# Kernel optimization log

Measured on AMD Instinct MI355X. Metric: run time of the kernel, lower is better.

Reference implementation:

```python
import jax, jax.numpy as jnp
import numpy as np
import math

D_MODEL = 1024
N_HEADS = 16
D_K = D_MODEL // N_HEADS


def setup_inputs() -> dict:
    key = jax.random.key(0)
    ks = jax.random.split(key, 9)
    s = 1.0 / math.sqrt(D_MODEL)
    x = jax.random.normal(ks[0], (2, 2048, D_MODEL), dtype=jnp.float32)
    # nn.Linear stores weight as [out, in]; we store transposed [in, out] for x @ W
    Wq = jax.random.uniform(ks[1], (D_MODEL, D_MODEL), jnp.float32, -s, s)
    bq = jax.random.uniform(ks[2], (D_MODEL,), jnp.float32, -s, s)
    Wk = jax.random.uniform(ks[3], (D_MODEL, D_MODEL), jnp.float32, -s, s)
    bk = jax.random.uniform(ks[4], (D_MODEL,), jnp.float32, -s, s)
    Wv = jax.random.uniform(ks[5], (D_MODEL, D_MODEL), jnp.float32, -s, s)
    bv = jax.random.uniform(ks[6], (D_MODEL,), jnp.float32, -s, s)
    Wo = jax.random.uniform(ks[7], (D_MODEL, D_MODEL), jnp.float32, -s, s)
    bo = jax.random.uniform(ks[8], (D_MODEL,), jnp.float32, -s, s)
    return {"x": x, "Wq": Wq, "bq": bq, "Wk": Wk, "bk": bk,
            "Wv": Wv, "bv": bv, "Wo": Wo, "bo": bo}


def reference(x, Wq, bq, Wk, bk, Wv, bv, Wo, bo):
    B, S, _ = x.shape
    scale = 1.0 / math.sqrt(D_K)
    # projections -> [B, H, S, Dk]
    def split_heads(t):
        return t.reshape(B, S, N_HEADS, D_K).transpose(0, 2, 1, 3)
    q = split_heads(x @ Wq + bq)
    k = split_heads(x @ Wk + bk)
    v = split_heads(x @ Wv + bv)
    # [B, H, S, S] scores
    scores = jnp.einsum('bhqd,bhkd->bhqk', q, k) * scale
    weights = jax.nn.softmax(scores, axis=-1)  # dropout p=0.0 -> identity
    attn = jnp.einsum('bhqk,bhkd->bhqd', weights, v)
    attn = attn.transpose(0, 2, 1, 3).reshape(B, S, D_MODEL)
    return attn @ Wo + bo
```

## Files before the change

kernel.cpp:

```cpp
#include <hip/hip_runtime.h>

#define DM    1024
#define NTOK  4096

typedef __attribute__((ext_vector_type(8))) short short8;
typedef __attribute__((ext_vector_type(4))) float floatx4;

__device__ __forceinline__ ushort f2bf(float f) {
  union { float f; uint32_t u; } v; v.f = f;
  uint32_t r = (v.u + 0x7fffu + ((v.u >> 16) & 1u)) >> 16;
  return (ushort)r;
}
__device__ __forceinline__ uint f2bf2(float a, float b) {
  return (uint)f2bf(a) | ((uint)f2bf(b) << 16);
}
__device__ __forceinline__ uint pkhi(float a, float b) {
  uint ua = __float_as_uint(a) + 0x8000u;
  uint ub = __float_as_uint(b) + 0x8000u;
  return __builtin_amdgcn_perm(ub, ua, 0x07060302);
}

__device__ __forceinline__ floatx4 mfma16(short8 a, short8 b, floatx4 c) {
  return __builtin_amdgcn_mfma_f32_16x16x32_bf16(a, b, c, 0, 0, 0);
}

__device__ __forceinline__ void glld16(const ushort* g, ushort* l) {
  __builtin_amdgcn_global_load_lds(
      (const __attribute__((address_space(1))) void*)g,
      (__attribute__((address_space(3))) void*)l, 16, 0, 0);
}

__device__ __forceinline__ void stage_slab(const ushort* gbase, int strideHW,
                                           ushort* lds, int ii, int lane) {
  const int r = ii * 8 + (lane >> 3);
  const int c = (lane & 7) ^ (r & 7);
  glld16(gbase + (size_t)r * strideHW + c * 8, lds + ii * 512);
}

__device__ __forceinline__ short8 fragr(const ushort* lds, int row, int chunk) {
  return *reinterpret_cast<const short8*>(&lds[row * 64 + ((chunk ^ (row & 7)) << 3)]);
}

__global__ __launch_bounds__(256) void k_prep(const float* __restrict__ x,
                                              const float* __restrict__ Wq,
                                              const float* __restrict__ Wk,
                                              const float* __restrict__ Wv,
                                              const float* __restrict__ Wo,
                                              ushort* __restrict__ xb,
                                              ushort* __restrict__ Wtout) {
  __shared__ float tile[32][33];
  const int bx = blockIdx.x, tid = threadIdx.x;
  if (bx < 2048) {
    int i = (bx * 256 + tid) * 8;
    float4 f0 = *reinterpret_cast<const float4*>(x + i);
    float4 f1 = *reinterpret_cast<const float4*>(x + i + 4);
    short8 o;
    o[0] = (short)f2bf(f0.x); o[1] = (short)f2bf(f0.y);
    o[2] = (short)f2bf(f0.z); o[3] = (short)f2bf(f0.w);
    o[4] = (short)f2bf(f1.x); o[5] = (short)f2bf(f1.y);
    o[6] = (short)f2bf(f1.z); o[7] = (short)f2bf(f1.w);
    *reinterpret_cast<short8*>(xb + i) = o;
    return;
  }
  const int idx = bx - 2048;
  const int z = idx >> 10, rem = idx & 1023;
  const float* W = (z == 0) ? Wq : (z == 1) ? Wk : (z == 2) ? Wv : Wo;
  ushort* Wt = Wtout + (size_t)z * (DM * DM);
  const int bxt = (rem & 31) * 32, byt = (rem >> 5) * 32;
  const int tx = tid & 31, ty = tid >> 5;
#pragma unroll
  for (int i = 0; i < 32; i += 8)
    tile[ty + i][tx] = W[(byt + ty + i) * DM + bxt + tx];
  __syncthreads();
#pragma unroll
  for (int i = 0; i < 32; i += 8)
    Wt[(bxt + ty + i) * DM + byt + tx] = f2bf(tile[tx][ty + i]);
}

__global__ __launch_bounds__(256) void k_gemm_qkv(const ushort* __restrict__ Am,
                                                  const ushort* __restrict__ Bm,
                                                  const float* __restrict__ bq,
                                                  const float* __restrict__ bk,
                                                  const float* __restrict__ bv,
                                                  ushort* __restrict__ Qo,
                                                  ushort* __restrict__ Ko,
                                                  ushort* __restrict__ Vto) {
  __shared__ ushort smem[32768];
  const int tid = threadIdx.x;
  const int w = tid >> 6, lane = tid & 63;
  const int quad = lane >> 4, l15 = lane & 15;
  const int wm = w >> 1, wn = w & 1;
  const int bm = blockIdx.x & 31, bn = blockIdx.x >> 5;
  const int sel = bn >> 3;
  const int bnl = bn & 7;

  const ushort* Ab = Am + (size_t)bm * 128 * 1024;
  const ushort* Bb = Bm + (size_t)bn * 128 * 1024;

  floatx4 acc[4][4] = {};

  auto stage = [&](int it, int buf) {
    ushort* As = smem + buf * 16384;
    ushort* Bs = As + 8192;
    const int k0 = it * 64;
#pragma unroll
    for (int i = 0; i < 4; ++i) stage_slab(Ab + k0, 1024, As, w * 4 + i, lane);
#pragma unroll
    for (int i = 0; i < 4; ++i) stage_slab(Bb + k0, 1024, Bs, w * 4 + i, lane);
  };

  stage(0, 0);
  for (int it = 0; it < 16; ++it) {
    __syncthreads();
    if (it + 1 < 16) stage(it + 1, (it + 1) & 1);
    const ushort* As = smem + (it & 1) * 16384;
    const ushort* Bs = As + 8192;
#pragma unroll
    for (int ks = 0; ks < 2; ++ks) {
      short8 af[4], bf[4];
#pragma unroll
      for (int t = 0; t < 4; ++t) {
        af[t] = fragr(As, wm * 64 + t * 16 + l15, ks * 4 + quad);
        bf[t] = fragr(Bs, wn * 64 + t * 16 + l15, ks * 4 + quad);
      }
#pragma unroll
      for (int tm = 0; tm < 4; ++tm)
#pragma unroll
        for (int tn = 0; tn < 4; ++tn)
          acc[tm][tn] = mfma16(af[tm], bf[tn], acc[tm][tn]);
    }
  }

  if (sel < 2) {
    const float* bp = sel ? bk : bq;
    ushort* dst = sel ? Ko : Qo;
    const float sc = sel ? 1.0f : 0.18033688f;
#pragma unroll
    for (int tm = 0; tm < 4; ++tm)
#pragma unroll
      for (int tn = 0; tn < 4; ++tn) {
        const int mg0 = bm * 128 + wm * 64 + tm * 16 + quad * 4;
        const int np = bnl * 128 + wn * 64 + tn * 16 + l15;
        const float bb = bp[np];
#pragma unroll
        for (int r = 0; r < 4; ++r) {
          const int m = mg0 + r;
          float v = (acc[tm][tn][r] + bb) * sc;
          dst[(size_t)((m >> 11) * 16 + (np >> 6)) * 131072 + (m & 2047) * 64 + (np & 63)] = f2bf(v);
        }
      }
  } else {
    __syncthreads();
    ushort* T = smem;
#pragma unroll
    for (int tm = 0; tm < 4; ++tm)
#pragma unroll
      for (int tn = 0; tn < 4; ++tn) {
        const int ml = wm * 64 + tm * 16 + quad * 4;
        const int nl = wn * 64 + tn * 16 + l15;
        const float bb = bv[bnl * 128 + nl];
        uint p0 = f2bf2(acc[tm][tn][0] + bb, acc[tm][tn][1] + bb);
        uint p1 = f2bf2(acc[tm][tn][2] + bb, acc[tm][tn][3] + bb);
        *reinterpret_cast<uint*>(&T[nl * 136 + ml]) = p0;
        *reinterpret_cast<uint*>(&T[nl * 136 + ml + 2]) = p1;
      }
    __syncthreads();
    const int tok0 = bm * 128;
    const int b = tok0 >> 11, s0 = tok0 & 2047;
    const int col = (tid & 15) * 8;
#pragma unroll
    for (int i = 0; i < 8; ++i) {
      const int rowl = i * 16 + (tid >> 4);
      const int dp = bnl * 128 + rowl;
      const int h = dp >> 6, d = dp & 63;
      *reinterpret_cast<int4*>(Vto + (size_t)((b * 16 + h) * 64 + d) * 2048 + s0 + col) =
          *reinterpret_cast<int4*>(&T[rowl * 136 + col]);
    }
  }
}

__global__ __launch_bounds__(256) void k_gemm_out(const ushort* __restrict__ Am,
                                                  const ushort* __restrict__ Bm,
                                                  const float* __restrict__ bias,
                                                  float* __restrict__ outp) {
  __shared__ ushort smem[24576];
  const int tid = threadIdx.x;
  const int w = tid >> 6, lane = tid & 63;
  const int quad = lane >> 4, l15 = lane & 15;
  const int wm = w >> 1, wn = w & 1;
  const int bm = blockIdx.x >> 3, bn = blockIdx.x & 7;

  const ushort* Ab = Am + (size_t)bm * 64 * 1024;
  const ushort* Bb = Bm + (size_t)bn * 128 * 1024;

  floatx4 acc[2][4] = {};

  auto stage = [&](int it, int buf) {
    ushort* As = smem + buf * 12288;
    ushort* Bs = As + 4096;
    const int k0 = it * 64;
#pragma unroll
    for (int i = 0; i < 2; ++i) stage_slab(Ab + k0, 1024, As, w * 2 + i, lane);
#pragma unroll
    for (int i = 0; i < 4; ++i) stage_slab(Bb + k0, 1024, Bs, w * 4 + i, lane);
  };

  stage(0, 0);
  for (int it = 0; it < 16; ++it) {
    __syncthreads();
    if (it + 1 < 16) stage(it + 1, (it + 1) & 1);
    const ushort* As = smem + (it & 1) * 12288;
    const ushort* Bs = As + 4096;
#pragma unroll
    for (int ks = 0; ks < 2; ++ks) {
      short8 af[2], bf[4];
#pragma unroll
      for (int t = 0; t < 2; ++t)
        af[t] = fragr(As, wm * 32 + t * 16 + l15, ks * 4 + quad);
#pragma unroll
      for (int t = 0; t < 4; ++t)
        bf[t] = fragr(Bs, wn * 64 + t * 16 + l15, ks * 4 + quad);
#pragma unroll
      for (int tm = 0; tm < 2; ++tm)
#pragma unroll
        for (int tn = 0; tn < 4; ++tn)
          acc[tm][tn] = mfma16(af[tm], bf[tn], acc[tm][tn]);
    }
  }

#pragma unroll
  for (int tm = 0; tm < 2; ++tm)
#pragma unroll
    for (int tn = 0; tn < 4; ++tn) {
      const int mg0 = bm * 64 + wm * 32 + tm * 16 + quad * 4;
      const int ng = bn * 128 + wn * 64 + tn * 16 + l15;
      const float bb = bias[ng];
#pragma unroll
      for (int r = 0; r < 4; ++r)
        outp[(size_t)(mg0 + r) * 1024 + ng] = acc[tm][tn][r] + bb;
    }
}

__global__ __launch_bounds__(256) void k_attn(const ushort* __restrict__ Q,
                                              const ushort* __restrict__ Kc,
                                              const ushort* __restrict__ Vt,
                                              ushort* __restrict__ attnb) {
  __shared__ ushort KV[2][8192];
  const int tid = threadIdx.x;
  const int w = tid >> 6, lane = tid & 63;
  const int quad = lane >> 4, l15 = lane & 15;
  const int bx = blockIdx.x;
  const int bh = (bx & 7) * 4 + ((bx >> 3) & 3);
  const int qc = bx >> 5;
  const int qt0 = qc * 128 + w * 32;
  const ushort* Qb = Q + (size_t)bh * 131072;
  const ushort* Kp = Kc + (size_t)bh * 131072;
  const ushort* Vp = Vt + (size_t)bh * 131072;

  short8 qf[2][2];
#pragma unroll
  for (int qs = 0; qs < 2; ++qs)
#pragma unroll
    for (int ks = 0; ks < 2; ++ks)
      qf[qs][ks] = *reinterpret_cast<const short8*>(
          Qb + (size_t)(qt0 + qs * 16 + l15) * 64 + ks * 32 + quad * 8);

  const int krho8 = lane >> 3;
  const int vt_ = (lane & 7) ^ (lane >> 3);

  auto stage = [&](int kt, int buf) {
    const int c = w & 1;
    ushort* dst = &KV[buf][(w >> 1) * 4096 + c * 2048];
    const int kc = kt * 64 + c * 32;
    if (w < 2) {
#pragma unroll
      for (int si = 0; si < 4; ++si) {
        const int rho = si * 8 + krho8;
        const int g = ((rho >> 2) & 3) * 8 + ((rho >> 4) & 1) * 4 + (rho & 3);
        const int cc = (lane & 7) ^ (rho & 7);
        glld16(Kp + (size_t)(kc + g) * 64 + cc * 8, dst + si * 512);
      }
    } else {
#pragma unroll
      for (int si = 0; si < 4; ++si) {
        const int d = (si * 8 + krho8) * 2 + (vt_ >> 2);
        glld16(Vp + (size_t)d * 2048 + kc + (vt_ & 3) * 8, dst + si * 512);
      }
    }
  };

  floatx4 oaccT[2][4] = {};
  floatx4 lacc[2] = {};

  auto computeChunk = [&](const ushort* Kb, const ushort* Vb) {
    floatx4 st[2][2] = {};
#pragma unroll
    for (int ks = 0; ks < 2; ++ks) {
      short8 kf0 = fragr(Kb, l15, ks * 4 + quad);
      short8 kf1 = fragr(Kb, 16 + l15, ks * 4 + quad);
      st[0][0] = mfma16(kf0, qf[0][ks], st[0][0]);
      st[0][1] = mfma16(kf1, qf[0][ks], st[0][1]);
      st[1][0] = mfma16(kf0, qf[1][ks], st[1][0]);
      st[1][1] = mfma16(kf1, qf[1][ks], st[1][1]);
    }
    short8 vf[4];
#pragma unroll
    for (int tn = 0; tn < 4; ++tn) {
      const int pg = tn * 8 + (l15 >> 1);
      const int cc = ((l15 & 1) * 4 + quad) ^ (l15 >> 1);
      vf[tn] = *reinterpret_cast<const short8*>(&Vb[pg * 64 + cc * 8]);
    }
#pragma unroll
    for (int qs = 0; qs < 2; ++qs) {
      floatx4 p0, p1;
#pragma unroll
      for (int r = 0; r < 4; ++r) {
        p0[r] = __builtin_amdgcn_exp2f(st[qs][0][r]);
        p1[r] = __builtin_amdgcn_exp2f(st[qs][1][r]);
      }
      lacc[qs] += p0;
      lacc[qs] += p1;
      union { uint4 u; short8 s; } pb;
      pb.u = (uint4){pkhi(p0[0], p0[1]), pkhi(p0[2], p0[3]),
                     pkhi(p1[0], p1[1]), pkhi(p1[2], p1[3])};
#pragma unroll
      for (int tn = 0; tn < 4; ++tn)
        oaccT[qs][tn] = mfma16(vf[tn], pb.s, oaccT[qs][tn]);
    }
  };

  stage(0, 0);
  for (int kt = 0; kt < 32; ++kt) {
    __syncthreads();
    if (kt + 1 < 32) stage(kt + 1, (kt + 1) & 1);
    const ushort* buf = KV[kt & 1];
    computeChunk(buf, buf + 4096);
    computeChunk(buf + 2048, buf + 6144);
  }

  float linv[2];
#pragma unroll
  for (int qs = 0; qs < 2; ++qs) {
    float l = lacc[qs][0] + lacc[qs][1] + lacc[qs][2] + lacc[qs][3];
    l += __shfl_xor(l, 16);
    l += __shfl_xor(l, 32);
    linv[qs] = 1.0f / l;
  }

  const int b = bh >> 4, h = bh & 15;
#pragma unroll
  for (int qs = 0; qs < 2; ++qs) {
    const int tok = b * 2048 + qt0 + qs * 16 + l15;
#pragma unroll
    for (int tn = 0; tn < 4; ++tn) {
      float v0 = oaccT[qs][tn][0] * linv[qs];
      float v1 = oaccT[qs][tn][1] * linv[qs];
      float v2 = oaccT[qs][tn][2] * linv[qs];
      float v3 = oaccT[qs][tn][3] * linv[qs];
      ushort* p = attnb + (size_t)tok * 1024 + h * 64 + tn * 16 + quad * 4;
      *reinterpret_cast<uint*>(p) = pkhi(v0, v1);
      *reinterpret_cast<uint*>(p + 2) = pkhi(v2, v3);
    }
  }
}

extern "C" void kernel_launch(void* const* d_in, const int* in_sizes, int n_in,
                              void* d_out, int out_size, void* d_ws, size_t ws_size,
                              hipStream_t stream) {
  const float* x  = (const float*)d_in[0];
  const float* Wq = (const float*)d_in[1];
  const float* bq = (const float*)d_in[2];
  const float* Wk = (const float*)d_in[3];
  const float* bk = (const float*)d_in[4];
  const float* Wv = (const float*)d_in[5];
  const float* bv = (const float*)d_in[6];
  const float* Wo = (const float*)d_in[7];
  const float* bo = (const float*)d_in[8];

  ushort* ws = (ushort*)d_ws;
  ushort* xb    = ws;
  ushort* Wqt   = ws + 4194304;
  ushort* Wot   = ws + 7340032;
  ushort* Qb    = ws + 8388608;
  ushort* Kbuf  = ws + 12582912;
  ushort* Vtb   = ws + 16777216;
  ushort* attnb = ws + 20971520;

  k_prep<<<6144, 256, 0, stream>>>(x, Wq, Wk, Wv, Wo, xb, Wqt);
  k_gemm_qkv<<<768, 256, 0, stream>>>(xb, Wqt, bq, bk, bv, Qb, Kbuf, Vtb);
  k_attn<<<512, 256, 0, stream>>>(Qb, Kbuf, Vtb, attnb);
  k_gemm_out<<<512, 256, 0, stream>>>(attnb, Wot, bo, (float*)d_out);
}
```

Baseline: 183.6 us.

## Widen weight-transpose tiles and double attention K/V stage size per barrier

The weight transpose in the prep kernel now uses 64x64 tiles with float4 loads and bf16 conversion before LDS, then writes 16-byte vectors. This cuts the block count and makes global stores wide. The attention kernel now stages 128 keys per double-buffer step instead of 64, halving the number of barriers and loop iterations. The cost is twice the LDS for K/V (64KB), which may lower occupancy for the attention blocks.

```diff
diff --git a/kernel.cpp b/kernel.cpp
--- a/kernel.cpp
+++ b/kernel.cpp
@@ -48,7 +48,7 @@
                                               const float* __restrict__ Wo,
                                               ushort* __restrict__ xb,
                                               ushort* __restrict__ Wtout) {
-  __shared__ float tile[32][33];
+  __shared__ ushort T[64 * 72];
   const int bx = blockIdx.x, tid = threadIdx.x;
   if (bx < 2048) {
     int i = (bx * 256 + tid) * 8;
@@ -63,18 +63,27 @@
     return;
   }
   const int idx = bx - 2048;
-  const int z = idx >> 10, rem = idx & 1023;
+  const int z = idx >> 8, rem = idx & 255;
   const float* W = (z == 0) ? Wq : (z == 1) ? Wk : (z == 2) ? Wv : Wo;
   ushort* Wt = Wtout + (size_t)z * (DM * DM);
-  const int bxt = (rem & 31) * 32, byt = (rem >> 5) * 32;
-  const int tx = tid & 31, ty = tid >> 5;
-#pragma unroll
-  for (int i = 0; i < 32; i += 8)
-    tile[ty + i][tx] = W[(byt + ty + i) * DM + bxt + tx];
+  const int br = (rem >> 4) * 64;
+  const int bc = (rem & 15) * 64;
+  const int tr = tid >> 2;
+  const int tc = (tid & 3) * 16;
+
+  const float* src = W + (size_t)(br + tr) * DM + bc + tc;
+#pragma unroll
+  for (int j = 0; j < 4; ++j) {
+    float4 v = *reinterpret_cast<const float4*>(src + j * 4);
+    T[(tc + j * 4 + 0) * 72 + tr] = f2bf(v.x);
+    T[(tc + j * 4 + 1) * 72 + tr] = f2bf(v.y);
+    T[(tc + j * 4 + 2) * 72 + tr] = f2bf(v.z);
+    T[(tc + j * 4 + 3) * 72 + tr] = f2bf(v.w);
+  }
   __syncthreads();
-#pragma unroll
-  for (int i = 0; i < 32; i += 8)
-    Wt[(bxt + ty + i) * DM + byt + tx] = f2bf(tile[tx][ty + i]);
+  ushort* dst = Wt + (size_t)(bc + tr) * DM + br + tc;
+  *reinterpret_cast<int4*>(dst) = *reinterpret_cast<const int4*>(&T[tr * 72 + tc]);
+  *reinterpret_cast<int4*>(dst + 8) = *reinterpret_cast<const int4*>(&T[tr * 72 + tc + 8]);
 }
 
 __global__ __launch_bounds__(256) void k_gemm_qkv(const ushort* __restrict__ Am,
@@ -245,7 +254,7 @@
                                               const ushort* __restrict__ Kc,
                                               const ushort* __restrict__ Vt,
                                               ushort* __restrict__ attnb) {
-  __shared__ ushort KV[2][8192];
+  __shared__ ushort KV[2][16384];
   const int tid = threadIdx.x;
   const int w = tid >> 6, lane = tid & 63;
   const int quad = lane >> 4, l15 = lane & 15;
@@ -269,22 +278,26 @@
   const int vt_ = (lane & 7) ^ (lane >> 3);
 
   auto stage = [&](int kt, int buf) {
-    const int c = w & 1;
-    ushort* dst = &KV[buf][(w >> 1) * 4096 + c * 2048];
-    const int kc = kt * 64 + c * 32;
-    if (w < 2) {
-#pragma unroll
-      for (int si = 0; si < 4; ++si) {
-        const int rho = si * 8 + krho8;
-        const int g = ((rho >> 2) & 3) * 8 + ((rho >> 4) & 1) * 4 + (rho & 3);
-        const int cc = (lane & 7) ^ (rho & 7);
-        glld16(Kp + (size_t)(kc + g) * 64 + cc * 8, dst + si * 512);
-      }
-    } else {
-#pragma unroll
-      for (int si = 0; si < 4; ++si) {
-        const int d = (si * 8 + krho8) * 2 + (vt_ >> 2);
-        glld16(Vp + (size_t)d * 2048 + kc + (vt_ & 3) * 8, dst + si * 512);
+#pragma unroll
+    for (int i = 0; i < 2; ++i) {
+      const int sub = (w & 1) * 2 + i;
+      const int kc = kt * 128 + sub * 32;
+      if (w < 2) {
+        ushort* dst = &KV[buf][sub * 2048];
+#pragma unroll
+        for (int si = 0; si < 4; ++si) {
+          const int rho = si * 8 + krho8;
+          const int g = ((rho >> 2) & 3) * 8 + ((rho >> 4) & 1) * 4 + (rho & 3);
+          const int cc = (lane & 7) ^ (rho & 7);
+          glld16(Kp + (size_t)(kc + g) * 64 + cc * 8, dst + si * 512);
+        }
+      } else {
+        ushort* dst = &KV[buf][8192 + sub * 2048];
+#pragma unroll
+        for (int si = 0; si < 4; ++si) {
+          const int d = (si * 8 + krho8) * 2 + (vt_ >> 2);
+          glld16(Vp + (size_t)d * 2048 + kc + (vt_ & 3) * 8, dst + si * 512);
+        }
       }
     }
   };
@@ -330,12 +343,13 @@
   };
 
   stage(0, 0);
-  for (int kt = 0; kt < 32; ++kt) {
+  for (int kt = 0; kt < 16; ++kt) {
     __syncthreads();
-    if (kt + 1 < 32) stage(kt + 1, (kt + 1) & 1);
+    if (kt + 1 < 16) stage(kt + 1, (kt + 1) & 1);
     const ushort* buf = KV[kt & 1];
-    computeChunk(buf, buf + 4096);
-    computeChunk(buf + 2048, buf + 6144);
+#pragma unroll
+    for (int c = 0; c < 4; ++c)
+      computeChunk(buf + c * 2048, buf + 8192 + c * 2048);
   }
 
   float linv[2];
@@ -386,7 +400,7 @@
   ushort* Vtb   = ws + 16777216;
   ushort* attnb = ws + 20971520;
 
-  k_prep<<<6144, 256, 0, stream>>>(x, Wq, Wk, Wv, Wo, xb, Wqt);
+  k_prep<<<3072, 256, 0, stream>>>(x, Wq, Wk, Wv, Wo, xb, Wqt);
   k_gemm_qkv<<<768, 256, 0, stream>>>(xb, Wqt, bq, bk, bv, Qb, Kbuf, Vtb);
   k_attn<<<512, 256, 0, stream>>>(Qb, Kbuf, Vtb, attnb);
   k_gemm_out<<<512, 256, 0, stream>>>(attnb, Wot, bo, (float*)d_out);
```

New measurement: 183.6 us. Within noise of the previous version (+0.0%).
